# Performance work log

Hardware: AMD Instinct MI355X
Metric: run time of the kernel (lower is better)

The kernel has to match this reference:

```python
import jax, jax.numpy as jnp
import numpy as np

N_NODES = 50000
N_EDGES = 800000
D = 64
L = 2
EPS = 1e-9


def setup_inputs() -> dict:
    key = jax.random.key(0)
    ks = jax.random.split(key, 8)
    node_feats = jax.random.normal(ks[0], (N_NODES, D), dtype=jnp.float32)
    edge_src = jax.random.randint(ks[1], (N_EDGES,), 0, N_NODES, dtype=jnp.int32)
    edge_dst = jnp.sort(jax.random.randint(ks[2], (N_EDGES,), 0, N_NODES, dtype=jnp.int32))
    edge_w = jax.random.uniform(ks[3], (N_EDGES,), dtype=jnp.float32)
    W0 = jax.random.normal(ks[4], (D, D), dtype=jnp.float32) / np.sqrt(D)
    b0 = jax.random.normal(ks[5], (D,), dtype=jnp.float32) * 0.02
    W1 = jax.random.normal(ks[6], (D, D), dtype=jnp.float32) / np.sqrt(D)
    b1 = jax.random.normal(ks[7], (D,), dtype=jnp.float32) * 0.02
    return {"node_feats": node_feats, "edge_src": edge_src, "edge_dst": edge_dst,
            "edge_w": edge_w, "W0": W0, "b0": b0, "W1": W1, "b1": b1}


def reference(node_feats, edge_src, edge_dst, edge_w, W0, b0, W1, b1):
    n = node_feats.shape[0]
    # per-destination normalizer: sum of incoming edge weights + eps
    denom = jax.ops.segment_sum(edge_w, edge_dst, num_segments=n) + EPS  # [N]
    feats = node_feats
    for _ in range(L):
        # gather neighbor feats, weight, scatter-add to destination, normalize
        weighted = edge_w[:, None] * feats[edge_src]                      # [E, D]
        msg = jax.ops.segment_sum(weighted, edge_dst, num_segments=n)     # [N, D]
        msg = msg / denom[:, None]
        feats = jax.nn.relu(feats @ W0.T + b0 + msg @ W1.T + b1)
        # isolated nodes: segment_sum gives 0 -> msg = 0, matching msg=0.0 in torch
    return feats
```

## Files before the change

kernel.cpp:

```cpp
#include <hip/hip_runtime.h>

#define D 64
#define EPSV 1e-9f

typedef __attribute__((ext_vector_type(8))) short bf8_t;
typedef __attribute__((ext_vector_type(4))) float f4_t;

__device__ inline float bf2f(short u) {
    union { unsigned int i; float f; } v;
    v.i = ((unsigned int)(unsigned short)u) << 16;
    return v.f;
}
__device__ inline unsigned short f2bf(float f) {
    union { float f; unsigned int i; } v; v.f = f;
    unsigned int r = v.i + 0x7fff + ((v.i >> 16) & 1);
    return (unsigned short)(r >> 16);
}

__global__ void prep_kernel(const float* __restrict__ node_feats,
                            const int*   __restrict__ edge_dst,
                            const float* __restrict__ W0,
                            const float* __restrict__ W1,
                            int* __restrict__ row_off,
                            unsigned short* __restrict__ Wpack,
                            unsigned short* __restrict__ X,
                            int n_nodes, int n_edges, int cvtb)
{
    const int bid = blockIdx.x;
    const int tid = threadIdx.x;
    if (bid < cvtb) {
        const int i = bid * 256 + tid;
        if (i < n_nodes * 16) {
            const float4 v = ((const float4*)node_feats)[i];
            const int row = i >> 4, c4 = (i & 15) * 4;
            unsigned short* p = X + row * 64 + c4;
            p[0] = f2bf(v.x); p[1] = f2bf(v.y); p[2] = f2bf(v.z); p[3] = f2bf(v.w);
        }
    } else if (bid < cvtb + 32) {
        const int idx = (bid - cvtb) * 256 + tid;
        const int j = idx & 7, lane = (idx >> 3) & 63, kk = (idx >> 9) & 3, t = idx >> 11;
        const int k = kk * 32 + (lane >> 4) * 8 + j;
        const int d = t * 16 + (lane & 15);
        const float v = (k < D) ? W0[d * D + k] : W1[d * D + (k - D)];
        Wpack[idx] = f2bf(v);
    } else {
        const int n = (bid - cvtb - 32) * 256 + tid;
        if (n <= n_nodes) {
            int lo = 0, hi = n_edges;
            while (lo < hi) {
                const int mid = (lo + hi) >> 1;
                if (edge_dst[mid] < n) lo = mid + 1; else hi = mid;
            }
            row_off[n] = lo;
        }
    }
}

template<int OUT_F32>
__global__ __launch_bounds__(256, 4) void layer_kernel(
    const unsigned short* __restrict__ Xin,
    const int*   __restrict__ row_off,
    const int*   __restrict__ edge_src,
    const float* __restrict__ edge_w,
    const unsigned short* __restrict__ Wpack,
    const float* __restrict__ b0,
    const float* __restrict__ b1,
    void* __restrict__ outp,
    int n_nodes)
{
    __shared__ __align__(16) unsigned short lds_msg[16][72];

    const int lane = threadIdx.x & 63;
    const int w    = threadIdx.x >> 6;
    const int rowbase = blockIdx.x * 16;

    const int nb = rowbase + w * 4;
    int s[4], e[4];
    #pragma unroll
    for (int i = 0; i < 4; ++i) {
        int n = nb + i; if (n >= n_nodes) n = n_nodes - 1;
        s[i] = row_off[n]; e[i] = row_off[n + 1];
    }
    int dmax = 0;
    #pragma unroll
    for (int i = 0; i < 4; ++i) { const int d = e[i] - s[i]; if (d > dmax) dmax = d; }

    const int slot = lane >> 3;
    const int fo   = (lane & 7) * 8;

    float acc[4][8];
    float ws[4];
    #pragma unroll
    for (int i = 0; i < 4; ++i) {
        ws[i] = 0.f;
        #pragma unroll
        for (int m = 0; m < 8; ++m) acc[i][m] = 0.f;
    }

    for (int base = 0; base < dmax; base += 16) {
        #pragma unroll
        for (int i = 0; i < 4; ++i) {
            const int  ej0 = s[i] + base + slot;
            const int  ej1 = ej0 + 8;
            const bool v0 = ej0 < e[i], v1 = ej1 < e[i];
            const float w0 = v0 ? edge_w[ej0] : 0.f;
            const float w1 = v1 ? edge_w[ej1] : 0.f;
            const int  sc0 = v0 ? edge_src[ej0] : 0;
            const int  sc1 = v1 ? edge_src[ej1] : 0;
            const bf8_t f0 = *(const bf8_t*)(Xin + sc0 * 64 + fo);
            const bf8_t f1 = *(const bf8_t*)(Xin + sc1 * 64 + fo);
            #pragma unroll
            for (int m = 0; m < 8; ++m)
                acc[i][m] = fmaf(w0, bf2f(f0[m]), fmaf(w1, bf2f(f1[m]), acc[i][m]));
            ws[i] += w0 + w1;
        }
    }

    #pragma unroll
    for (int off = 8; off <= 32; off <<= 1) {
        #pragma unroll
        for (int i = 0; i < 4; ++i) {
            #pragma unroll
            for (int m = 0; m < 8; ++m) acc[i][m] += __shfl_xor(acc[i][m], off);
            ws[i] += __shfl_xor(ws[i], off);
        }
    }

    const int g = lane >> 3;
    #pragma unroll
    for (int i = 0; i < 4; ++i) {
        if (g == i) {
            const float inv = 1.0f / (ws[i] + EPSV);
            bf8_t mv;
            #pragma unroll
            for (int m = 0; m < 8; ++m) mv[m] = (short)f2bf(acc[i][m] * inv);
            *(bf8_t*)(&lds_msg[w * 4 + i][fo]) = mv;
        }
    }

    __syncthreads();

    bf8_t bfr[4];
    #pragma unroll
    for (int kk = 0; kk < 4; ++kk)
        bfr[kk] = *(const bf8_t*)(Wpack + ((w * 4 + kk) * 64 + lane) * 8);

    const int arow16 = lane & 15;
    const int koff   = (lane >> 4) * 8;
    int arow = rowbase + arow16; if (arow >= n_nodes) arow = n_nodes - 1;
    const unsigned short* ap = Xin + arow * 64 + koff;

    bf8_t af[4];
    af[0] = *(const bf8_t*)(ap);
    af[1] = *(const bf8_t*)(ap + 32);
    af[2] = *(const bf8_t*)(&lds_msg[arow16][koff]);
    af[3] = *(const bf8_t*)(&lds_msg[arow16][koff + 32]);

    f4_t acc4 = (f4_t){0.f, 0.f, 0.f, 0.f};
    #pragma unroll
    for (int kk = 0; kk < 4; ++kk)
        acc4 = __builtin_amdgcn_mfma_f32_16x16x32_bf16(af[kk], bfr[kk], acc4, 0, 0, 0);

    const int col  = w * 16 + (lane & 15);
    const float bias = b0[col] + b1[col];
    #pragma unroll
    for (int r = 0; r < 4; ++r) {
        const int row = rowbase + (lane >> 4) * 4 + r;
        if (row < n_nodes) {
            const float v = fmaxf(acc4[r] + bias, 0.0f);
            if (OUT_F32) ((float*)outp)[row * 64 + col] = v;
            else ((unsigned short*)outp)[row * 64 + col] = f2bf(v);
        }
    }
}

extern "C" void kernel_launch(void* const* d_in, const int* in_sizes, int n_in,
                              void* d_out, int out_size, void* d_ws, size_t ws_size,
                              hipStream_t stream) {
    const float* node_feats = (const float*)d_in[0];
    const int*   edge_src   = (const int*)  d_in[1];
    const int*   edge_dst   = (const int*)  d_in[2];
    const float* edge_w     = (const float*)d_in[3];
    const float* W0         = (const float*)d_in[4];
    const float* b0         = (const float*)d_in[5];
    const float* W1         = (const float*)d_in[6];
    const float* b1         = (const float*)d_in[7];

    const int n_nodes = in_sizes[0] / D;
    const int n_edges = in_sizes[1];

    char* ws = (char*)d_ws;
    int*            row_off = (int*)ws;
    unsigned short* Wpack   = (unsigned short*)(ws + 204800);
    unsigned short* X0      = (unsigned short*)(ws + 237568);
    unsigned short* X1      = (unsigned short*)(ws + 237568 + 6400000);

    const int cvtb = (n_nodes * 16 + 255) / 256;
    const int offb = (n_nodes + 1 + 255) / 256;
    prep_kernel<<<cvtb + 32 + offb, 256, 0, stream>>>(node_feats, edge_dst, W0, W1,
                                                      row_off, Wpack, X0,
                                                      n_nodes, n_edges, cvtb);

    const int ntiles = (n_nodes + 15) / 16;

    layer_kernel<0><<<ntiles, 256, 0, stream>>>(X0, row_off, edge_src, edge_w,
                                                Wpack, b0, b1, X1, n_nodes);
    layer_kernel<1><<<ntiles, 256, 0, stream>>>(X1, row_off, edge_src, edge_w,
                                                Wpack, b0, b1, d_out, n_nodes);
}
```

Before: 75.49 us.

## Split fused layer into separate aggregate and persistent MFMA GEMM kernels

Replaces the fused per-layer kernel with two kernels: a gather-aggregate kernel that writes normalized bf16 messages to a workspace buffer, and a persistent-grid MFMA GEMM in which each wave holds all weight fragments and loops over 16-row tiles. The aggregation also preloads the first 32 edges per node up front to expose more memory-level parallelism, and uses readfirstlane for the node index. This removes the block-wide LDS sync and per-block weight reload, but adds a round trip of the message matrix through global memory and two extra kernel launches.

```diff
diff --git a/kernel.cpp b/kernel.cpp
--- a/kernel.cpp
+++ b/kernel.cpp
@@ -56,38 +56,40 @@
     }
 }
 
-template<int OUT_F32>
-__global__ __launch_bounds__(256, 4) void layer_kernel(
+__global__ __launch_bounds__(256, 4) void aggregate_kernel(
     const unsigned short* __restrict__ Xin,
+    unsigned short* __restrict__ M,
     const int*   __restrict__ row_off,
     const int*   __restrict__ edge_src,
     const float* __restrict__ edge_w,
-    const unsigned short* __restrict__ Wpack,
-    const float* __restrict__ b0,
-    const float* __restrict__ b1,
-    void* __restrict__ outp,
     int n_nodes)
 {
-    __shared__ __align__(16) unsigned short lds_msg[16][72];
-
     const int lane = threadIdx.x & 63;
-    const int w    = threadIdx.x >> 6;
-    const int rowbase = blockIdx.x * 16;
-
-    const int nb = rowbase + w * 4;
+    const int wib  = threadIdx.x >> 6;
+    const int nb   = (blockIdx.x * 4 + wib) * 4;
+
     int s[4], e[4];
     #pragma unroll
     for (int i = 0; i < 4; ++i) {
         int n = nb + i; if (n >= n_nodes) n = n_nodes - 1;
+        n = __builtin_amdgcn_readfirstlane(n);
         s[i] = row_off[n]; e[i] = row_off[n + 1];
     }
-    int dmax = 0;
-    #pragma unroll
-    for (int i = 0; i < 4; ++i) { const int d = e[i] - s[i]; if (d > dmax) dmax = d; }
 
     const int slot = lane >> 3;
     const int fo   = (lane & 7) * 8;
 
+    float wM[4][4]; int sM[4][4];
+    #pragma unroll
+    for (int i = 0; i < 4; ++i)
+        #pragma unroll
+        for (int g = 0; g < 4; ++g) {
+            const int  ej = s[i] + g * 8 + slot;
+            const bool v  = ej < e[i];
+            wM[i][g] = v ? edge_w[ej] : 0.f;
+            sM[i][g] = v ? edge_src[ej] : 0;
+        }
+
     float acc[4][8];
     float ws[4];
     #pragma unroll
@@ -97,7 +99,21 @@
         for (int m = 0; m < 8; ++m) acc[i][m] = 0.f;
     }
 
-    for (int base = 0; base < dmax; base += 16) {
+    #pragma unroll
+    for (int i = 0; i < 4; ++i)
+        #pragma unroll
+        for (int g = 0; g < 4; ++g) {
+            const bf8_t f = *(const bf8_t*)(Xin + sM[i][g] * 64 + fo);
+            #pragma unroll
+            for (int m = 0; m < 8; ++m)
+                acc[i][m] = fmaf(wM[i][g], bf2f(f[m]), acc[i][m]);
+            ws[i] += wM[i][g];
+        }
+
+    int dmax = 0;
+    #pragma unroll
+    for (int i = 0; i < 4; ++i) { const int d = e[i] - s[i]; if (d > dmax) dmax = d; }
+    for (int base = 32; base < dmax; base += 16) {
         #pragma unroll
         for (int i = 0; i < 4; ++i) {
             const int  ej0 = s[i] + base + slot;
@@ -130,46 +146,81 @@
     #pragma unroll
     for (int i = 0; i < 4; ++i) {
         if (g == i) {
-            const float inv = 1.0f / (ws[i] + EPSV);
-            bf8_t mv;
-            #pragma unroll
-            for (int m = 0; m < 8; ++m) mv[m] = (short)f2bf(acc[i][m] * inv);
-            *(bf8_t*)(&lds_msg[w * 4 + i][fo]) = mv;
-        }
-    }
-
-    __syncthreads();
-
-    bf8_t bfr[4];
-    #pragma unroll
-    for (int kk = 0; kk < 4; ++kk)
-        bfr[kk] = *(const bf8_t*)(Wpack + ((w * 4 + kk) * 64 + lane) * 8);
-
-    const int arow16 = lane & 15;
-    const int koff   = (lane >> 4) * 8;
-    int arow = rowbase + arow16; if (arow >= n_nodes) arow = n_nodes - 1;
-    const unsigned short* ap = Xin + arow * 64 + koff;
-
-    bf8_t af[4];
-    af[0] = *(const bf8_t*)(ap);
-    af[1] = *(const bf8_t*)(ap + 32);
-    af[2] = *(const bf8_t*)(&lds_msg[arow16][koff]);
-    af[3] = *(const bf8_t*)(&lds_msg[arow16][koff + 32]);
-
-    f4_t acc4 = (f4_t){0.f, 0.f, 0.f, 0.f};
-    #pragma unroll
-    for (int kk = 0; kk < 4; ++kk)
-        acc4 = __builtin_amdgcn_mfma_f32_16x16x32_bf16(af[kk], bfr[kk], acc4, 0, 0, 0);
-
-    const int col  = w * 16 + (lane & 15);
-    const float bias = b0[col] + b1[col];
-    #pragma unroll
-    for (int r = 0; r < 4; ++r) {
-        const int row = rowbase + (lane >> 4) * 4 + r;
-        if (row < n_nodes) {
-            const float v = fmaxf(acc4[r] + bias, 0.0f);
-            if (OUT_F32) ((float*)outp)[row * 64 + col] = v;
-            else ((unsigned short*)outp)[row * 64 + col] = f2bf(v);
+            int n = nb + i; if (n < n_nodes) {
+                const float inv = 1.0f / (ws[i] + EPSV);
+                bf8_t mv;
+                #pragma unroll
+                for (int m = 0; m < 8; ++m) mv[m] = (short)f2bf(acc[i][m] * inv);
+                *(bf8_t*)(M + n * 64 + fo) = mv;
+            }
+        }
+    }
+}
+
+template<int OUT_F32>
+__global__ __launch_bounds__(256, 4) void gemm_mfma(
+    const unsigned short* __restrict__ X,
+    const unsigned short* __restrict__ M,
+    const unsigned short* __restrict__ Wpack,
+    const float* __restrict__ b0,
+    const float* __restrict__ b1,
+    void* __restrict__ outp,
+    int ntiles, int waves_total, int n_nodes)
+{
+    const int lane = threadIdx.x & 63;
+    const int wib  = threadIdx.x >> 6;
+    const int wave = __builtin_amdgcn_readfirstlane(blockIdx.x * 4 + wib);
+
+    bf8_t bfr[4][4];
+    #pragma unroll
+    for (int t = 0; t < 4; ++t)
+        #pragma unroll
+        for (int kk = 0; kk < 4; ++kk)
+            bfr[t][kk] = *(const bf8_t*)(Wpack + ((t * 4 + kk) * 64 + lane) * 8);
+
+    float bias[4];
+    #pragma unroll
+    for (int t = 0; t < 4; ++t) {
+        const int col = t * 16 + (lane & 15);
+        bias[t] = b0[col] + b1[col];
+    }
+
+    const int koff = (lane >> 4) * 8;
+
+    for (int tile = wave; tile < ntiles; tile += waves_total) {
+        const int rowbase = tile * 16;
+        int arow = rowbase + (lane & 15); if (arow >= n_nodes) arow = n_nodes - 1;
+        const unsigned short* ap = X + arow * 64 + koff;
+        const unsigned short* mp = M + arow * 64 + koff;
+
+        bf8_t af[4];
+        af[0] = *(const bf8_t*)(ap);
+        af[1] = *(const bf8_t*)(ap + 32);
+        af[2] = *(const bf8_t*)(mp);
+        af[3] = *(const bf8_t*)(mp + 32);
+
+        f4_t acc[4];
+        #pragma unroll
+        for (int t = 0; t < 4; ++t) acc[t] = (f4_t){0.f, 0.f, 0.f, 0.f};
+
+        #pragma unroll
+        for (int t = 0; t < 4; ++t)
+            #pragma unroll
+            for (int kk = 0; kk < 4; ++kk)
+                acc[t] = __builtin_amdgcn_mfma_f32_16x16x32_bf16(af[kk], bfr[t][kk], acc[t], 0, 0, 0);
+
+        #pragma unroll
+        for (int t = 0; t < 4; ++t) {
+            const int col = t * 16 + (lane & 15);
+            #pragma unroll
+            for (int r = 0; r < 4; ++r) {
+                const int row = rowbase + (lane >> 4) * 4 + r;
+                if (row < n_nodes) {
+                    const float v = fmaxf(acc[t][r] + bias[t], 0.0f);
+                    if (OUT_F32) ((float*)outp)[row * 64 + col] = v;
+                    else ((unsigned short*)outp)[row * 64 + col] = f2bf(v);
+                }
+            }
         }
     }
 }
@@ -194,6 +245,7 @@
     unsigned short* Wpack   = (unsigned short*)(ws + 204800);
     unsigned short* X0      = (unsigned short*)(ws + 237568);
     unsigned short* X1      = (unsigned short*)(ws + 237568 + 6400000);
+    unsigned short* M       = (unsigned short*)(ws + 237568 + 12800000);
 
     const int cvtb = (n_nodes * 16 + 255) / 256;
     const int offb = (n_nodes + 1 + 255) / 256;
@@ -201,10 +253,13 @@
                                                       row_off, Wpack, X0,
                                                       n_nodes, n_edges, cvtb);
 
+    const int agrid  = (n_nodes + 15) / 16;
     const int ntiles = (n_nodes + 15) / 16;
-
-    layer_kernel<0><<<ntiles, 256, 0, stream>>>(X0, row_off, edge_src, edge_w,
-                                                Wpack, b0, b1, X1, n_nodes);
-    layer_kernel<1><<<ntiles, 256, 0, stream>>>(X1, row_off, edge_src, edge_w,
-                                                Wpack, b0, b1, d_out, n_nodes);
-}
+    const int ggrid  = 256;
+    const int gwaves = ggrid * 4;
+
+    aggregate_kernel<<<agrid, 256, 0, stream>>>(X0, M, row_off, edge_src, edge_w, n_nodes);
+    gemm_mfma<0><<<ggrid, 256, 0, stream>>>(X0, M, Wpack, b0, b1, X1, ntiles, gwaves, n_nodes);
+    aggregate_kernel<<<agrid, 256, 0, stream>>>(X1, M, row_off, edge_src, edge_w, n_nodes);
+    gemm_mfma<1><<<ggrid, 256, 0, stream>>>(X1, M, Wpack, b0, b1, d_out, ntiles, gwaves, n_nodes);
+}
```

After: 84.37 us. 1.12x slower.

## Remap aggregation to one node per 16-lane group and build CSR by edge scan

Applied to the files above, without the earlier changes.

Row offsets are now built by scanning edges and filling the gaps between consecutive destinations, replacing a per-node binary search. Each wavefront now gives every node its own 16-lane quarter, with two edge slots per quarter, instead of looping over four nodes with all lanes. Edges are gathered in batches of four, with the first 16 edges unconditionally unrolled, so more loads are in flight. Occupancy hint raised to 6 blocks per CU. The change cuts shuffle reductions and per-node serialization, but per-lane loop trip counts now follow the highest-degree node among the four a wave handles, and the edge-scan writes can be imbalanced across gaps.

```diff
diff --git a/kernel.cpp b/kernel.cpp
--- a/kernel.cpp
+++ b/kernel.cpp
@@ -26,8 +26,7 @@
                             unsigned short* __restrict__ X,
                             int n_nodes, int n_edges, int cvtb)
 {
-    const int bid = blockIdx.x;
-    const int tid = threadIdx.x;
+    const int bid = blockIdx.x, tid = threadIdx.x;
     if (bid < cvtb) {
         const int i = bid * 256 + tid;
         if (i < n_nodes * 16) {
@@ -44,20 +43,42 @@
         const float v = (k < D) ? W0[d * D + k] : W1[d * D + (k - D)];
         Wpack[idx] = f2bf(v);
     } else {
-        const int n = (bid - cvtb - 32) * 256 + tid;
-        if (n <= n_nodes) {
-            int lo = 0, hi = n_edges;
-            while (lo < hi) {
-                const int mid = (lo + hi) >> 1;
-                if (edge_dst[mid] < n) lo = mid + 1; else hi = mid;
-            }
-            row_off[n] = lo;
+        const int i = (bid - cvtb - 32) * 256 + tid;
+        if (i <= n_edges) {
+            const int prev = (i == 0) ? -1 : edge_dst[i - 1];
+            const int cur  = (i == n_edges) ? n_nodes : edge_dst[i];
+            for (int n = prev + 1; n <= cur; ++n) row_off[n] = i;
         }
     }
 }
 
+__device__ __forceinline__ void agg_batch8(
+    const unsigned short* __restrict__ X,
+    const int* __restrict__ edge_src, const float* __restrict__ edge_w,
+    int s, int e, int b, int slot, int fo,
+    float acc[8], float& wsum)
+{
+    float w[4]; int sc[4];
+    #pragma unroll
+    for (int r = 0; r < 4; ++r) {
+        const int  ej = s + b + r * 2 + slot;
+        const bool v  = ej < e;
+        w[r]  = v ? edge_w[ej] : 0.f;
+        sc[r] = v ? edge_src[ej] : 0;
+    }
+    bf8_t f[4];
+    #pragma unroll
+    for (int r = 0; r < 4; ++r) f[r] = *(const bf8_t*)(X + sc[r] * 64 + fo);
+    #pragma unroll
+    for (int r = 0; r < 4; ++r) {
+        #pragma unroll
+        for (int m = 0; m < 8; ++m) acc[m] = fmaf(w[r], bf2f(f[r][m]), acc[m]);
+        wsum += w[r];
+    }
+}
+
 template<int OUT_F32>
-__global__ __launch_bounds__(256, 4) void layer_kernel(
+__global__ __launch_bounds__(256, 6) void layer_fused(
     const unsigned short* __restrict__ Xin,
     const int*   __restrict__ row_off,
     const int*   __restrict__ edge_src,
@@ -74,68 +95,45 @@
     const int w    = threadIdx.x >> 6;
     const int rowbase = blockIdx.x * 16;
 
-    const int nb = rowbase + w * 4;
-    int s[4], e[4];
-    #pragma unroll
-    for (int i = 0; i < 4; ++i) {
-        int n = nb + i; if (n >= n_nodes) n = n_nodes - 1;
-        s[i] = row_off[n]; e[i] = row_off[n + 1];
-    }
-    int dmax = 0;
-    #pragma unroll
-    for (int i = 0; i < 4; ++i) { const int d = e[i] - s[i]; if (d > dmax) dmax = d; }
-
-    const int slot = lane >> 3;
+    const int q    = lane >> 4;
+    const int slot = (lane >> 3) & 1;
     const int fo   = (lane & 7) * 8;
 
-    float acc[4][8];
-    float ws[4];
-    #pragma unroll
-    for (int i = 0; i < 4; ++i) {
-        ws[i] = 0.f;
+    int node = rowbase + w * 4 + q;
+    if (node >= n_nodes) node = n_nodes - 1;
+    const int s = row_off[node];
+    const int e = row_off[node + 1];
+    const int deg = e - s;
+    int dm = deg;
+    dm = max(dm, __shfl_xor(dm, 16));
+    dm = max(dm, __shfl_xor(dm, 32));
+
+    float acc[8];
+    #pragma unroll
+    for (int m = 0; m < 8; ++m) acc[m] = 0.f;
+    float wsum = 0.f;
+
+    agg_batch8(Xin, edge_src, edge_w, s, e, 0, slot, fo, acc, wsum);
+    agg_batch8(Xin, edge_src, edge_w, s, e, 8, slot, fo, acc, wsum);
+    if (dm > 16) {
+        agg_batch8(Xin, edge_src, edge_w, s, e, 16, slot, fo, acc, wsum);
+        agg_batch8(Xin, edge_src, edge_w, s, e, 24, slot, fo, acc, wsum);
+    }
+    for (int base = 32; base < dm; base += 16) {
+        agg_batch8(Xin, edge_src, edge_w, s, e, base, slot, fo, acc, wsum);
+        agg_batch8(Xin, edge_src, edge_w, s, e, base + 8, slot, fo, acc, wsum);
+    }
+
+    #pragma unroll
+    for (int m = 0; m < 8; ++m) acc[m] += __shfl_xor(acc[m], 8);
+    wsum += __shfl_xor(wsum, 8);
+
+    if ((lane & 8) == 0) {
+        const float inv = 1.0f / (wsum + EPSV);
+        bf8_t mv;
         #pragma unroll
-        for (int m = 0; m < 8; ++m) acc[i][m] = 0.f;
-    }
-
-    for (int base = 0; base < dmax; base += 16) {
-        #pragma unroll
-        for (int i = 0; i < 4; ++i) {
-            const int  ej0 = s[i] + base + slot;
-            const int  ej1 = ej0 + 8;
-            const bool v0 = ej0 < e[i], v1 = ej1 < e[i];
-            const float w0 = v0 ? edge_w[ej0] : 0.f;
-            const float w1 = v1 ? edge_w[ej1] : 0.f;
-            const int  sc0 = v0 ? edge_src[ej0] : 0;
-            const int  sc1 = v1 ? edge_src[ej1] : 0;
-            const bf8_t f0 = *(const bf8_t*)(Xin + sc0 * 64 + fo);
-            const bf8_t f1 = *(const bf8_t*)(Xin + sc1 * 64 + fo);
-            #pragma unroll
-            for (int m = 0; m < 8; ++m)
-                acc[i][m] = fmaf(w0, bf2f(f0[m]), fmaf(w1, bf2f(f1[m]), acc[i][m]));
-            ws[i] += w0 + w1;
-        }
-    }
-
-    #pragma unroll
-    for (int off = 8; off <= 32; off <<= 1) {
-        #pragma unroll
-        for (int i = 0; i < 4; ++i) {
-            #pragma unroll
-            for (int m = 0; m < 8; ++m) acc[i][m] += __shfl_xor(acc[i][m], off);
-            ws[i] += __shfl_xor(ws[i], off);
-        }
-    }
-
-    const int g = lane >> 3;
-    #pragma unroll
-    for (int i = 0; i < 4; ++i) {
-        if (g == i) {
-            const float inv = 1.0f / (ws[i] + EPSV);
-            bf8_t mv;
-            #pragma unroll
-            for (int m = 0; m < 8; ++m) mv[m] = (short)f2bf(acc[i][m] * inv);
-            *(bf8_t*)(&lds_msg[w * 4 + i][fo]) = mv;
-        }
+        for (int m = 0; m < 8; ++m) mv[m] = (short)f2bf(acc[m] * inv);
+        *(bf8_t*)(&lds_msg[w * 4 + q][fo]) = mv;
     }
 
     __syncthreads();
@@ -148,11 +146,10 @@
     const int arow16 = lane & 15;
     const int koff   = (lane >> 4) * 8;
     int arow = rowbase + arow16; if (arow >= n_nodes) arow = n_nodes - 1;
-    const unsigned short* ap = Xin + arow * 64 + koff;
 
     bf8_t af[4];
-    af[0] = *(const bf8_t*)(ap);
-    af[1] = *(const bf8_t*)(ap + 32);
+    af[0] = *(const bf8_t*)(Xin + arow * 64 + koff);
+    af[1] = *(const bf8_t*)(Xin + arow * 64 + 32 + koff);
     af[2] = *(const bf8_t*)(&lds_msg[arow16][koff]);
     af[3] = *(const bf8_t*)(&lds_msg[arow16][koff + 32]);
 
@@ -169,7 +166,7 @@
         if (row < n_nodes) {
             const float v = fmaxf(acc4[r] + bias, 0.0f);
             if (OUT_F32) ((float*)outp)[row * 64 + col] = v;
-            else ((unsigned short*)outp)[row * 64 + col] = f2bf(v);
+            else         ((unsigned short*)outp)[row * 64 + col] = f2bf(v);
         }
     }
 }
@@ -192,19 +189,20 @@
     char* ws = (char*)d_ws;
     int*            row_off = (int*)ws;
     unsigned short* Wpack   = (unsigned short*)(ws + 204800);
-    unsigned short* X0      = (unsigned short*)(ws + 237568);
-    unsigned short* X1      = (unsigned short*)(ws + 237568 + 6400000);
+    const size_t base = 237568;
+    unsigned short* X0 = (unsigned short*)(ws + base);
+    unsigned short* X1 = (unsigned short*)(ws + base + 6400000);
 
     const int cvtb = (n_nodes * 16 + 255) / 256;
-    const int offb = (n_nodes + 1 + 255) / 256;
+    const int offb = (n_edges + 1 + 255) / 256;
     prep_kernel<<<cvtb + 32 + offb, 256, 0, stream>>>(node_feats, edge_dst, W0, W1,
                                                       row_off, Wpack, X0,
                                                       n_nodes, n_edges, cvtb);
 
     const int ntiles = (n_nodes + 15) / 16;
 
-    layer_kernel<0><<<ntiles, 256, 0, stream>>>(X0, row_off, edge_src, edge_w,
-                                                Wpack, b0, b1, X1, n_nodes);
-    layer_kernel<1><<<ntiles, 256, 0, stream>>>(X1, row_off, edge_src, edge_w,
-                                                Wpack, b0, b1, d_out, n_nodes);
-}
+    layer_fused<0><<<ntiles, 256, 0, stream>>>(X0, row_off, edge_src, edge_w,
+                                               Wpack, b0, b1, X1, n_nodes);
+    layer_fused<1><<<ntiles, 256, 0, stream>>>(X1, row_off, edge_src, edge_w,
+                                               Wpack, b0, b1, d_out, n_nodes);
+}
```

Measured after the change: 69.93 us. -7.4%, faster.
